# Kernel tuning notes

Measured on AMD Instinct MI355X. Metric: run time of the kernel, lower is better.

Reference implementation:

```python
import jax, jax.numpy as jnp
import numpy as np
import math

NUM_EXPERTS = 64
CAPACITY_FACTOR = 1.0


def reference(x, wg):
    # x: [S, D] tokens, wg: [E, D] router weight (torch Linear layout)
    S, D = x.shape
    E = wg.shape[0]
    capacity = int(CAPACITY_FACTOR * math.ceil(S / E))  # training-mode capacity

    logits = jnp.einsum('sd,ed->se', x, wg)              # [S, E]
    gates = jax.nn.softmax(logits, axis=1)               # [S, E]

    indices1_s = jnp.argmax(gates, axis=1)               # [S]
    mask1 = jax.nn.one_hot(indices1_s, E, dtype=gates.dtype)  # [S, E]

    gates1_s = jnp.sum(gates * mask1, axis=1)            # [S]
    locations1 = jnp.cumsum(mask1, axis=0) - 1.0         # fused_cumsum_sub_one, [S, E]

    # load-balancing auxiliary loss
    me = jnp.mean(gates, axis=0)                         # [E]
    ce = jnp.mean(mask1, axis=0)                         # [E]
    l_aux = jnp.mean(me * ce) * (E * E)

    # drop tokens over capacity
    mask1 = mask1 * (locations1 < capacity).astype(mask1.dtype)
    locations1_s = jnp.sum(locations1 * mask1, axis=1).astype(jnp.int32)  # [S]

    gates1 = gates1_s[:, None] * mask1                   # [S, E]
    locations1_sc = jax.nn.one_hot(locations1_s, capacity, dtype=gates1.dtype)  # [S, C]
    # bmm(gates1[:, :, 1], locations1_sc[:, 1, :]) -> outer product per token
    combine1_sec = gates1[:, :, None] * locations1_sc[:, None, :]  # [S, E, C]
    dispatch_mask = combine1_sec.astype(bool)
    return (l_aux, combine1_sec, dispatch_mask)


def setup_inputs() -> dict:
    key = jax.random.key(0)
    k1, k2 = jax.random.split(key)
    x = jax.random.normal(k1, (8192, 2048), dtype=jnp.float32)
    wg = jax.random.normal(k2, (NUM_EXPERTS, 2048), dtype=jnp.float32) * 0.02
    return {"x": x, "wg": wg}
```

## Files before the change

kernel.cpp:

```cpp
#include <hip/hip_runtime.h>
#include <cstdint>
#include <cstddef>

#define S_TOK 8192
#define DIM   2048
#define NE    64
#define CAP   128
#define KSPLIT 4
#define BS    64
#define DT    32
#define XW    36
#define WW    68

#define OFF_PART   0
#define OFF_IDX    2097152
#define OFF_GATE   2105344
#define OFF_LOC    2113536
#define OFF_MEPART 2121728
#define OFF_PROD   2154496

__global__ __launch_bounds__(256) void gemm_logits(
    const float* __restrict__ x, const float* __restrict__ wg,
    float* __restrict__ part)
{
    __shared__ float xs[BS][XW];
    __shared__ float wshT[DT][WW];

    const int sb  = blockIdx.x * BS;
    const int k   = blockIdx.y;
    const int d0  = k * (DIM / KSPLIT);
    const int tid = threadIdx.x;

    const int r = tid >> 3;
    const int c = (tid & 7) * 4;
    const int ti = tid >> 4;
    const int ei = tid & 15;

    float4 acc4[4];
    #pragma unroll
    for (int i = 0; i < 4; ++i) acc4[i] = make_float4(0.f, 0.f, 0.f, 0.f);

    for (int t = 0; t < DIM / KSPLIT; t += DT) {
        {
            const float4 xa = *reinterpret_cast<const float4*>(
                &x[(size_t)(sb + r) * DIM + d0 + t + c]);
            const float4 xb = *reinterpret_cast<const float4*>(
                &x[(size_t)(sb + r + 32) * DIM + d0 + t + c]);
            *reinterpret_cast<float4*>(&xs[r][c])      = xa;
            *reinterpret_cast<float4*>(&xs[r + 32][c]) = xb;
        }
        {
            const float4 w0 = *reinterpret_cast<const float4*>(
                &wg[(size_t)r * DIM + d0 + t + c]);
            const float4 w1 = *reinterpret_cast<const float4*>(
                &wg[(size_t)(r + 32) * DIM + d0 + t + c]);
            wshT[c + 0][r] = w0.x; wshT[c + 1][r] = w0.y;
            wshT[c + 2][r] = w0.z; wshT[c + 3][r] = w0.w;
            wshT[c + 0][r + 32] = w1.x; wshT[c + 1][r + 32] = w1.y;
            wshT[c + 2][r + 32] = w1.z; wshT[c + 3][r + 32] = w1.w;
        }
        __syncthreads();
        #pragma unroll
        for (int dq = 0; dq < DT / 4; ++dq) {
            float4 xv[4], wv[4];
            #pragma unroll
            for (int i = 0; i < 4; ++i)
                xv[i] = *reinterpret_cast<const float4*>(&xs[ti * 4 + i][dq * 4]);
            #pragma unroll
            for (int q = 0; q < 4; ++q)
                wv[q] = *reinterpret_cast<const float4*>(&wshT[dq * 4 + q][ei * 4]);
            #pragma unroll
            for (int i = 0; i < 4; ++i) {
                acc4[i].x += xv[i].x*wv[0].x + xv[i].y*wv[1].x + xv[i].z*wv[2].x + xv[i].w*wv[3].x;
                acc4[i].y += xv[i].x*wv[0].y + xv[i].y*wv[1].y + xv[i].z*wv[2].y + xv[i].w*wv[3].y;
                acc4[i].z += xv[i].x*wv[0].z + xv[i].y*wv[1].z + xv[i].z*wv[2].z + xv[i].w*wv[3].z;
                acc4[i].w += xv[i].x*wv[0].w + xv[i].y*wv[1].w + xv[i].z*wv[2].w + xv[i].w*wv[3].w;
            }
        }
        __syncthreads();
    }
    #pragma unroll
    for (int i = 0; i < 4; ++i)
        *reinterpret_cast<float4*>(
            &part[((size_t)k * S_TOK + sb + ti * 4 + i) * NE + ei * 4]) = acc4[i];
}

__global__ __launch_bounds__(256) void softmax_top1(
    const float* __restrict__ part, int* __restrict__ idx,
    float* __restrict__ gate, float* __restrict__ me_part)
{
    const int lane = threadIdx.x & 63;
    const int wid  = threadIdx.x >> 6;
    const int gw   = blockIdx.x * 4 + wid;

    float me_acc = 0.f;
    for (int s = gw; s < S_TOK; s += 512) {
        float l = 0.f;
        #pragma unroll
        for (int k = 0; k < KSPLIT; ++k)
            l += part[((size_t)k * S_TOK + s) * NE + lane];
        float m = l;
        #pragma unroll
        for (int o = 32; o; o >>= 1) m = fmaxf(m, __shfl_xor(m, o));
        const float ex = __expf(l - m);
        float sum = ex;
        #pragma unroll
        for (int o = 32; o; o >>= 1) sum += __shfl_xor(sum, o);
        float bv = l; int bi = lane;
        #pragma unroll
        for (int o = 32; o; o >>= 1) {
            const float ov = __shfl_xor(bv, o);
            const int   oi = __shfl_xor(bi, o);
            if (ov > bv || (ov == bv && oi < bi)) { bv = ov; bi = oi; }
        }
        const float g = ex / sum;
        me_acc += g;
        if (lane == bi) {
            idx[s]  = bi;
            gate[s] = g;
        }
    }
    me_part[(size_t)gw * NE + lane] = me_acc;
}

__global__ __launch_bounds__(256) void scan_expert(
    const int* __restrict__ idx, const float* __restrict__ me_part,
    int* __restrict__ loc, float* __restrict__ prod)
{
    const int e    = blockIdx.x;
    const int tid  = threadIdx.x;
    const int lane = tid & 63;
    const int wid  = tid >> 6;
    __shared__ int   wsum[4];
    __shared__ float redf[4];

    float mp = me_part[(size_t)tid * NE + e] + me_part[(size_t)(tid + 256) * NE + e];
    #pragma unroll
    for (int o = 32; o; o >>= 1) mp += __shfl_xor(mp, o);
    if (lane == 0) redf[wid] = mp;

    int running = 0;
    for (int c = 0; c < S_TOK; c += 256) {
        const int s = c + tid;
        const bool match = (idx[s] == e);
        const unsigned long long b = __ballot(match);
        const int before = __popcll(b & ((1ULL << lane) - 1ULL));
        if (lane == 0) wsum[wid] = __popcll(b);
        __syncthreads();
        int woff = 0;
        #pragma unroll
        for (int w = 0; w < 4; ++w) if (w < wid) woff += wsum[w];
        const int tot = wsum[0] + wsum[1] + wsum[2] + wsum[3];
        if (match) {
            const int pos = running + woff + before;
            loc[s] = (pos < CAP) ? pos : -1;
        }
        running += tot;
        __syncthreads();
    }
    if (tid == 0) {
        const float me = (redf[0] + redf[1] + redf[2] + redf[3]) / (float)S_TOK;
        const float ce = (float)running / (float)S_TOK;
        prod[e] = me * ce;
    }
}

__global__ __launch_bounds__(256) void zero_scatter(
    const int* __restrict__ idx, const int* __restrict__ loc,
    const float* __restrict__ gate, const float* __restrict__ prod,
    float* __restrict__ out)
{
    const int s   = blockIdx.x;
    const int tid = threadIdx.x;
    float* cslab = out + 1 + (size_t)s * (NE * CAP);
    float* dslab = cslab + (size_t)S_TOK * NE * CAP;

    const float4 z = {0.f, 0.f, 0.f, 0.f};
    if (tid < 3)        { cslab[tid]  = 0.f; dslab[tid]  = 0.f; }
    else if (tid == 3)  { cslab[8191] = 0.f; dslab[8191] = 0.f; }
    float4* cb = reinterpret_cast<float4*>(cslab + 3);
    float4* db = reinterpret_cast<float4*>(dslab + 3);
    #pragma unroll
    for (int j = tid; j < 2047; j += 256) { cb[j] = z; db[j] = z; }

    __syncthreads();

    if (tid == 0) {
        const int l = loc[s];
        if (l >= 0) {
            const int t = idx[s] * CAP + l;
            cslab[t] = gate[s];
            dslab[t] = 1.0f;
        }
    }
    if (s == 0 && tid >= 64 && tid < 128) {
        const int ln = tid - 64;
        float p = prod[ln];
        #pragma unroll
        for (int o = 32; o; o >>= 1) p += __shfl_xor(p, o);
        if (ln == 0) out[0] = p * (float)NE;
    }
}

extern "C" void kernel_launch(void* const* d_in, const int* in_sizes, int n_in,
                              void* d_out, int out_size, void* d_ws, size_t ws_size,
                              hipStream_t stream)
{
    const float* x  = (const float*)d_in[0];
    const float* wg = (const float*)d_in[1];
    float* out = (float*)d_out;
    float* ws  = (float*)d_ws;

    float* part    = ws + OFF_PART;
    int*   idx     = (int*)(ws + OFF_IDX);
    float* gate    = ws + OFF_GATE;
    int*   loc     = (int*)(ws + OFF_LOC);
    float* me_part = ws + OFF_MEPART;
    float* prod    = ws + OFF_PROD;

    dim3 ggrid(S_TOK / BS, KSPLIT);
    gemm_logits<<<ggrid, 256, 0, stream>>>(x, wg, part);
    softmax_top1<<<128, 256, 0, stream>>>(part, idx, gate, me_part);
    scan_expert<<<NE, 256, 0, stream>>>(idx, me_part, loc, prod);
    zero_scatter<<<S_TOK, 256, 0, stream>>>(idx, loc, gate, prod, out);
}
```

Before: 635.7 us.

## Fuse output zero-fill into logits GEMM and shrink scatter to a thin kernel

The bulk zero-fill of the large combine and dispatch output tensors moves out of the per-token scatter kernel and into the logits GEMM. Each GEMM block writes a contiguous, float4-aligned slice of the output every K-iteration, so these stores can overlap the GEMM's loads and math. The final kernel then only places one gate value and one mask entry per token and computes the aux loss, using one thread per token. The cost is more global-store traffic inside the GEMM, which may slow its compute phase or compete with its x loads for memory bandwidth.

```diff
diff --git a/kernel.cpp b/kernel.cpp
--- a/kernel.cpp
+++ b/kernel.cpp
@@ -12,6 +12,8 @@
 #define XW    36
 #define WW    68
 
+#define NOUT4 33554432ULL
+
 #define OFF_PART   0
 #define OFF_IDX    2097152
 #define OFF_GATE   2105344
@@ -19,9 +21,9 @@
 #define OFF_MEPART 2121728
 #define OFF_PROD   2154496
 
-__global__ __launch_bounds__(256) void gemm_logits(
+__global__ __launch_bounds__(256) void gemm_zero(
     const float* __restrict__ x, const float* __restrict__ wg,
-    float* __restrict__ part)
+    float* __restrict__ part, float* __restrict__ out)
 {
     __shared__ float xs[BS][XW];
     __shared__ float wshT[DT][WW];
@@ -30,17 +32,23 @@
     const int k   = blockIdx.y;
     const int d0  = k * (DIM / KSPLIT);
     const int tid = threadIdx.x;
+    const int bid = blockIdx.y * (S_TOK / BS) + blockIdx.x;
 
     const int r = tid >> 3;
     const int c = (tid & 7) * 4;
     const int ti = tid >> 4;
     const int ei = tid & 15;
 
+    float4* outv = reinterpret_cast<float4*>(out);
+    const size_t zbase = (size_t)bid * 65536 + tid;
+    const float4 z4 = make_float4(0.f, 0.f, 0.f, 0.f);
+
     float4 acc4[4];
     #pragma unroll
-    for (int i = 0; i < 4; ++i) acc4[i] = make_float4(0.f, 0.f, 0.f, 0.f);
-
-    for (int t = 0; t < DIM / KSPLIT; t += DT) {
+    for (int i = 0; i < 4; ++i) acc4[i] = z4;
+
+    int it = 0;
+    for (int t = 0; t < DIM / KSPLIT; t += DT, ++it) {
         {
             const float4 xa = *reinterpret_cast<const float4*>(
                 &x[(size_t)(sb + r) * DIM + d0 + t + c]);
@@ -60,6 +68,11 @@
             wshT[c + 2][r + 32] = w1.z; wshT[c + 3][r + 32] = w1.w;
         }
         __syncthreads();
+
+        #pragma unroll
+        for (int j = 0; j < 16; ++j)
+            outv[zbase + (size_t)(it * 16 + j) * 256] = z4;
+
         #pragma unroll
         for (int dq = 0; dq < DT / 4; ++dq) {
             float4 xv[4], wv[4];
@@ -79,6 +92,8 @@
         }
         __syncthreads();
     }
+    if (bid == 511 && tid == 255) out[4ULL * NOUT4] = 0.f;
+
     #pragma unroll
     for (int i = 0; i < 4; ++i)
         *reinterpret_cast<float4*>(
@@ -165,40 +180,23 @@
     }
 }
 
-__global__ __launch_bounds__(256) void zero_scatter(
+__global__ __launch_bounds__(256) void scatter_final(
     const int* __restrict__ idx, const int* __restrict__ loc,
     const float* __restrict__ gate, const float* __restrict__ prod,
     float* __restrict__ out)
 {
-    const int s   = blockIdx.x;
-    const int tid = threadIdx.x;
-    float* cslab = out + 1 + (size_t)s * (NE * CAP);
-    float* dslab = cslab + (size_t)S_TOK * NE * CAP;
-
-    const float4 z = {0.f, 0.f, 0.f, 0.f};
-    if (tid < 3)        { cslab[tid]  = 0.f; dslab[tid]  = 0.f; }
-    else if (tid == 3)  { cslab[8191] = 0.f; dslab[8191] = 0.f; }
-    float4* cb = reinterpret_cast<float4*>(cslab + 3);
-    float4* db = reinterpret_cast<float4*>(dslab + 3);
-    #pragma unroll
-    for (int j = tid; j < 2047; j += 256) { cb[j] = z; db[j] = z; }
-
-    __syncthreads();
-
-    if (tid == 0) {
-        const int l = loc[s];
-        if (l >= 0) {
-            const int t = idx[s] * CAP + l;
-            cslab[t] = gate[s];
-            dslab[t] = 1.0f;
-        }
-    }
-    if (s == 0 && tid >= 64 && tid < 128) {
-        const int ln = tid - 64;
-        float p = prod[ln];
+    const int s = blockIdx.x * 256 + threadIdx.x;
+    const int l = loc[s];
+    if (l >= 0) {
+        const size_t off = ((size_t)s * NE + idx[s]) * CAP + l;
+        out[1 + off] = gate[s];
+        out[1 + (size_t)S_TOK * NE * CAP + off] = 1.0f;
+    }
+    if (blockIdx.x == 0 && threadIdx.x < 64) {
+        float p = prod[threadIdx.x];
         #pragma unroll
         for (int o = 32; o; o >>= 1) p += __shfl_xor(p, o);
-        if (ln == 0) out[0] = p * (float)NE;
+        if (threadIdx.x == 0) out[0] = p * (float)NE;
     }
 }
 
@@ -219,8 +217,8 @@
     float* prod    = ws + OFF_PROD;
 
     dim3 ggrid(S_TOK / BS, KSPLIT);
-    gemm_logits<<<ggrid, 256, 0, stream>>>(x, wg, part);
+    gemm_zero<<<ggrid, 256, 0, stream>>>(x, wg, part, out);
     softmax_top1<<<128, 256, 0, stream>>>(part, idx, gate, me_part);
     scan_expert<<<NE, 256, 0, stream>>>(idx, me_part, loc, prod);
-    zero_scatter<<<S_TOK, 256, 0, stream>>>(idx, loc, gate, prod, out);
-}
+    scatter_final<<<S_TOK / 256, 256, 0, stream>>>(idx, loc, gate, prod, out);
+}
```

After: 626.9 us. About the same (-1.4%).
